# Optimization experiments

Hardware: AMD Instinct MI355X
Metric: run time of the kernel (lower is better)

Reference implementation:

```python
import jax, jax.numpy as jnp
import numpy as np

B, L, D, H = 2, 2048, 512, 8
HD = D // H  # head_dim used only for the concat/reshape trick


def setup_inputs() -> dict:
    key = jax.random.key(0)
    ks = jax.random.split(key, 7)
    s = 0.02  # small init so softmax isn't saturated
    return {
        "q": jax.random.normal(ks[0], (B, L, D), jnp.float32),
        "k": jax.random.normal(ks[1], (B, L, D), jnp.float32),
        "v": jax.random.normal(ks[2], (B, L, D), jnp.float32),
        # per-head full-width projections: W[h] is the nn.Linear weight [out,in]
        "Wq": jax.random.normal(ks[3], (H, D, D), jnp.float32) * s,
        "Wk": jax.random.normal(ks[4], (H, D, D), jnp.float32) * s,
        "Wv": jax.random.normal(ks[5], (H, D, D), jnp.float32) * s,
        # output_layer Linear(d_model*num_heads -> d_model, bias=False)
        "Wo": jax.random.normal(ks[6], (D, H * D), jnp.float32) * s,
    }


def reference(q, k, v, Wq, Wk, Wv, Wo):
    # Each head applies its own full d_model x d_model projections (Linear: x @ W^T)
    qh = jnp.einsum('bld,hed->bhle', q, Wq)  # [B,H,L,D]
    kh = jnp.einsum('bld,hed->bhle', k, Wk)
    vh = jnp.einsum('bld,hed->bhle', v, Wv)
    # scaled by sqrt(d_k) with d_k = d_model (as in the original code)
    scores = jnp.einsum('bhle,bhme->bhlm', qh, kh) / jnp.sqrt(jnp.float32(D))
    attn = jax.nn.softmax(scores, axis=-1)          # [B,H,L,L] (dropout = identity in eval)
    ctx = jnp.einsum('bhlm,bhme->bhle', attn, vh)   # [B,H,L,D]
    # torch: each head ctx [B,L,D] -> view(B,L,H,HD); cat over heads on last dim -> [B,L,H,H*HD]; flatten
    comb = ctx.reshape(B, H, L, H, HD).transpose(0, 2, 3, 1, 4).reshape(B, L, H * D)
    out = comb @ Wo.T                               # [B,L,D]
    return out, attn
```

## Files before the change

kernel.cpp:

```cpp
#include <hip/hip_runtime.h>
#include <cstdio>
#include <cstdint>


#define AS1 __attribute__((address_space(1)))
#define AS3 __attribute__((address_space(3)))

typedef __attribute__((ext_vector_type(8))) short bf16x8;
typedef __attribute__((ext_vector_type(4))) short short4v;
typedef __attribute__((ext_vector_type(4))) float f32x4;

constexpr int cB = 2, cH = 8, cL = 2048, cD = 512;
constexpr float SCORE_SCALE = 0.044194173824159216f;

__device__ __forceinline__ short f2bf(float f) {
  return __builtin_bit_cast(short, static_cast<__bf16>(f));
}

__device__ __forceinline__ void gload16(const void* g, void* l) {
  __builtin_amdgcn_global_load_lds((AS1 const void*)g, (AS3 void*)l, 16, 0, 0);
}

struct CvtArgs { const float4* s[7]; short4v* d[7]; };

__global__ __launch_bounds__(256) void cvt_all(CvtArgs a) {
  const int z = blockIdx.y;
  const int i = blockIdx.x * 256 + threadIdx.x;
  const float4 v = a.s[z][i];
  short4v o = { f2bf(v.x), f2bf(v.y), f2bf(v.z), f2bf(v.w) };
  a.d[z][i] = o;
}

enum { M_PROJ = 0, M_PROJV = 1, M_SCORES = 2, M_OUT = 3 };

template <int MODE>
__global__ __launch_bounds__(256) void gemm_nt(const short* __restrict__ Ap,
                                               const short* __restrict__ Bp,
                                               void* __restrict__ Cp,
                                               float2* __restrict__ Sp) {
  constexpr int K   = (MODE == M_OUT) ? 2048 : 512;
  constexpr int LDA = (MODE == M_OUT) ? 4096 : 512;
  constexpr int LDB = (MODE == M_OUT) ? 4096 : 512;

  __shared__ short As[128 * 32];
  __shared__ short Bs[128 * 32];

  const int t = threadIdx.x;
  const int lane = t & 63;
  const int wv = t >> 6;
  const int wm = wv >> 1, wn = wv & 1;
  const int z = blockIdx.z;

  size_t Aoff, Boff;
  if constexpr (MODE == M_PROJ || MODE == M_PROJV) {
    Aoff = (size_t)(z >> 3) * ((size_t)cL * cD);
    Boff = (size_t)(z & 7) * ((size_t)cD * cD);
  } else if constexpr (MODE == M_SCORES) {
    Aoff = (size_t)z * ((size_t)cL * cD);
    Boff = (size_t)z * ((size_t)cL * cD);
  } else {
    Aoff = (size_t)(z >> 1) * ((size_t)cL * 4096) + (size_t)(z & 1) * 2048;
    Boff = (size_t)(z & 1) * 2048;
  }

  const short* Ag0 = Ap + Aoff + (size_t)(blockIdx.y * 128) * LDA;
  const short* Bg0 = Bp + Boff + (size_t)(blockIdx.x * 128) * LDB;

  f32x4 acc[4][4];
#pragma unroll
  for (int i = 0; i < 4; ++i)
#pragma unroll
    for (int j = 0; j < 4; ++j) acc[i][j] = (f32x4){0.f, 0.f, 0.f, 0.f};

  for (int kt = 0; kt < K; kt += 32) {
    __syncthreads();
#pragma unroll
    for (int r = 0; r < 2; ++r) {
      const int cbase = r * 256 + wv * 64;
      const int c = cbase + lane;
      const int row = c >> 2, col = (c & 3) * 8;
      gload16(Ag0 + (size_t)row * LDA + kt + col, &As[cbase * 8]);
    }
#pragma unroll
    for (int r = 0; r < 2; ++r) {
      const int cbase = r * 256 + wv * 64;
      const int c = cbase + lane;
      const int row = c >> 2, col = (c & 3) * 8;
      gload16(Bg0 + (size_t)row * LDB + kt + col, &Bs[cbase * 8]);
    }
    __syncthreads();

    const int koff = (lane >> 4) * 8;
    const int ar = wm * 64 + (lane & 15);
    const int br = wn * 64 + (lane & 15);
    bf16x8 af[4], bfv[4];
#pragma unroll
    for (int i = 0; i < 4; ++i) af[i] = *(const bf16x8*)&As[(ar + i * 16) * 32 + koff];
#pragma unroll
    for (int j = 0; j < 4; ++j) bfv[j] = *(const bf16x8*)&Bs[(br + j * 16) * 32 + koff];
#pragma unroll
    for (int i = 0; i < 4; ++i)
#pragma unroll
      for (int j = 0; j < 4; ++j)
        acc[i][j] = __builtin_amdgcn_mfma_f32_16x16x32_bf16(af[i], bfv[j], acc[i][j], 0, 0, 0);
  }

  const int r0 = (lane >> 4) * 4;
  const int cc = lane & 15;
  const int rowbase = blockIdx.y * 128 + wm * 64 + r0;
  const int colbase = blockIdx.x * 128 + wn * 64 + cc;

  if constexpr (MODE == M_PROJ) {
    short* C = (short*)Cp + (size_t)z * ((size_t)cL * cD);
#pragma unroll
    for (int i = 0; i < 4; ++i)
#pragma unroll
      for (int j = 0; j < 4; ++j)
#pragma unroll
        for (int r = 0; r < 4; ++r)
          C[(size_t)(rowbase + i * 16 + r) * cD + (colbase + j * 16)] = f2bf(acc[i][j][r]);
  } else if constexpr (MODE == M_PROJV) {
    short* C = (short*)Cp + (size_t)z * ((size_t)cD * cL);
#pragma unroll
    for (int i = 0; i < 4; ++i)
#pragma unroll
      for (int j = 0; j < 4; ++j) {
        short4v o = { f2bf(acc[i][j][0]), f2bf(acc[i][j][1]),
                      f2bf(acc[i][j][2]), f2bf(acc[i][j][3]) };
        *(short4v*)&C[(size_t)(colbase + j * 16) * cL + (rowbase + i * 16)] = o;
      }
  } else if constexpr (MODE == M_SCORES) {
    float* C = (float*)Cp + (size_t)z * ((size_t)cL * cL);
    float2* ps = Sp + (size_t)z * ((size_t)cL * 32);
    const int pid = blockIdx.x * 2 + wn;
#pragma unroll
    for (int i = 0; i < 4; ++i) {
      float sv[4][4];
#pragma unroll
      for (int j = 0; j < 4; ++j)
#pragma unroll
        for (int r = 0; r < 4; ++r) sv[j][r] = acc[i][j][r] * SCORE_SCALE;
#pragma unroll
      for (int j = 0; j < 4; ++j)
#pragma unroll
        for (int r = 0; r < 4; ++r)
          C[(size_t)(rowbase + i * 16 + r) * cL + (colbase + j * 16)] = sv[j][r];
#pragma unroll
      for (int r = 0; r < 4; ++r) {
        float mx = fmaxf(fmaxf(sv[0][r], sv[1][r]), fmaxf(sv[2][r], sv[3][r]));
#pragma unroll
        for (int off = 1; off < 16; off <<= 1) mx = fmaxf(mx, __shfl_xor(mx, off, 64));
        float sm = __expf(sv[0][r] - mx) + __expf(sv[1][r] - mx) +
                   __expf(sv[2][r] - mx) + __expf(sv[3][r] - mx);
#pragma unroll
        for (int off = 1; off < 16; off <<= 1) sm += __shfl_xor(sm, off, 64);
        if ((lane & 15) == 0)
          ps[(size_t)(rowbase + i * 16 + r) * 32 + pid] = make_float2(mx, sm);
      }
    }
  } else {
    float* C = (float*)Cp + (size_t)((z & 1) * 2 + (z >> 1)) * ((size_t)cL * cD);
#pragma unroll
    for (int i = 0; i < 4; ++i)
#pragma unroll
      for (int j = 0; j < 4; ++j)
#pragma unroll
        for (int r = 0; r < 4; ++r)
          C[(size_t)(rowbase + i * 16 + r) * cD + (colbase + j * 16)] = acc[i][j][r];
  }
}

__global__ __launch_bounds__(256) void combine_stats(const float2* __restrict__ ps,
                                                     float2* __restrict__ stats) {
  const int row = blockIdx.x * 256 + threadIdx.x;
  const float2* p = ps + (size_t)row * 32;
  float m = -1e30f;
#pragma unroll
  for (int i = 0; i < 32; ++i) m = fmaxf(m, p[i].x);
  float l = 0.f;
#pragma unroll
  for (int i = 0; i < 32; ++i) l += p[i].y * __expf(p[i].x - m);
  stats[row] = make_float2(m, 1.0f / l);
}

__global__ __launch_bounds__(512) void fused_ctx(const short* __restrict__ vhT,
                                                 const float2* __restrict__ stats,
                                                 float* __restrict__ attn,
                                                 short* __restrict__ comb) {
  __shared__ short Bs[2][512 * 32];
  __shared__ short Pb[2][128 * 32];

  const int t = threadIdx.x;
  const int lane = t & 63;
  const int wv = t >> 6;
  const int wm = wv >> 2, wn = wv & 3;
  const int rowblk = blockIdx.x;
  const int z = blockIdx.y;

  const int trow = t >> 2;
  const int tcb = t & 3;
  const int tslot = tcb ^ ((trow >> 1) & 3);
  const int grow = rowblk * 128 + trow;
  float* sp = attn + ((size_t)z * cL + grow) * cL + tcb * 8;
  const float2 st = stats[(size_t)z * cL + grow];
  const float m = st.x, invl = st.y;

  const short* Bg = vhT + (size_t)z * ((size_t)cD * cL);

  f32x4 acc[4][8];
#pragma unroll
  for (int i = 0; i < 4; ++i)
#pragma unroll
    for (int j = 0; j < 8; ++j) acc[i][j] = (f32x4){0.f, 0.f, 0.f, 0.f};

  const int qk = lane >> 4;
  const int ar = wm * 64 + (lane & 15);
  const int br = wn * 128 + (lane & 15);

  auto stageB = [&](int nb, int kt) {
#pragma unroll
    for (int r = 0; r < 4; ++r) {
      const int cbase = r * 512 + wv * 64;
      const int c = cbase + lane;
      const int row = c >> 2;
      const int swcol = ((c & 3) ^ ((row >> 1) & 3)) * 8;
      gload16(Bg + (size_t)row * cL + kt + swcol, &Bs[nb][cbase * 8]);
    }
  };
  auto transform = [&](int ck, float4 v0, float4 v1) -> bf16x8 {
    float* dst = sp + ck * 32;
    const float p0 = __expf(v0.x - m) * invl;
    const float p1 = __expf(v0.y - m) * invl;
    const float p2 = __expf(v0.z - m) * invl;
    const float p3 = __expf(v0.w - m) * invl;
    const float p4 = __expf(v1.x - m) * invl;
    const float p5 = __expf(v1.y - m) * invl;
    const float p6 = __expf(v1.z - m) * invl;
    const float p7 = __expf(v1.w - m) * invl;
    *(float4*)(dst)     = make_float4(p0, p1, p2, p3);
    *(float4*)(dst + 4) = make_float4(p4, p5, p6, p7);
    bf16x8 pb = { f2bf(p0), f2bf(p1), f2bf(p2), f2bf(p3),
                  f2bf(p4), f2bf(p5), f2bf(p6), f2bf(p7) };
    return pb;
  };

  stageB(0, 0);
  float4 c0 = *(const float4*)(sp);
  float4 c1 = *(const float4*)(sp + 4);
  bf16x8 pb = transform(0, c0, c1);
  c0 = *(const float4*)(sp + 32);
  c1 = *(const float4*)(sp + 36);
  *(bf16x8*)&Pb[0][trow * 32 + tslot * 8] = pb;

  for (int k = 0; k < 63; ++k) {
    const int cb = k & 1, nb = cb ^ 1;
    pb = transform(k + 1, c0, c1);
    const int kc = (k + 2) & 63;
    c0 = *(const float4*)(sp + kc * 32);
    c1 = *(const float4*)(sp + kc * 32 + 4);
    asm volatile("s_waitcnt vmcnt(4) lgkmcnt(0)" ::: "memory");
    __builtin_amdgcn_sched_barrier(0);
    __builtin_amdgcn_s_barrier();
    __builtin_amdgcn_sched_barrier(0);
    *(bf16x8*)&Pb[nb][trow * 32 + tslot * 8] = pb;
    stageB(nb, (k + 1) * 32);
    __builtin_amdgcn_sched_barrier(0);
    bf16x8 af[4], bfv[8];
#pragma unroll
    for (int i = 0; i < 4; ++i) {
      const int rA = ar + i * 16;
      af[i] = *(const bf16x8*)&Pb[cb][rA * 32 + (qk ^ ((rA >> 1) & 3)) * 8];
    }
#pragma unroll
    for (int j = 0; j < 8; ++j) {
      const int rB = br + j * 16;
      bfv[j] = *(const bf16x8*)&Bs[cb][rB * 32 + (qk ^ ((rB >> 1) & 3)) * 8];
    }
    __builtin_amdgcn_s_setprio(1);
#pragma unroll
    for (int i = 0; i < 4; ++i)
#pragma unroll
      for (int j = 0; j < 8; ++j)
        acc[i][j] = __builtin_amdgcn_mfma_f32_16x16x32_bf16(af[i], bfv[j], acc[i][j], 0, 0, 0);
    __builtin_amdgcn_s_setprio(0);
  }

  asm volatile("s_waitcnt vmcnt(0) lgkmcnt(0)" ::: "memory");
  __builtin_amdgcn_sched_barrier(0);
  __builtin_amdgcn_s_barrier();
  __builtin_amdgcn_sched_barrier(0);
  {
    bf16x8 af[4], bfv[8];
#pragma unroll
    for (int i = 0; i < 4; ++i) {
      const int rA = ar + i * 16;
      af[i] = *(const bf16x8*)&Pb[1][rA * 32 + (qk ^ ((rA >> 1) & 3)) * 8];
    }
#pragma unroll
    for (int j = 0; j < 8; ++j) {
      const int rB = br + j * 16;
      bfv[j] = *(const bf16x8*)&Bs[1][rB * 32 + (qk ^ ((rB >> 1) & 3)) * 8];
    }
    __builtin_amdgcn_s_setprio(1);
#pragma unroll
    for (int i = 0; i < 4; ++i)
#pragma unroll
      for (int j = 0; j < 8; ++j)
        acc[i][j] = __builtin_amdgcn_mfma_f32_16x16x32_bf16(af[i], bfv[j], acc[i][j], 0, 0, 0);
    __builtin_amdgcn_s_setprio(0);
  }

  const int r0 = (lane >> 4) * 4;
  const int cc = lane & 15;
  short* C = comb + (size_t)(z >> 3) * ((size_t)cL * (cH * cD));
  const int h = z & 7;
  const int rowbase = rowblk * 128 + wm * 64 + r0;
#pragma unroll
  for (int i = 0; i < 4; ++i)
#pragma unroll
    for (int j = 0; j < 8; ++j) {
      const int e = wn * 128 + j * 16 + cc;
      const int jc = ((e >> 6) << 9) + (h << 6) + (e & 63);
#pragma unroll
      for (int r = 0; r < 4; ++r)
        C[(size_t)(rowbase + i * 16 + r) * (cH * cD) + jc] = f2bf(acc[i][j][r]);
    }
}

__global__ __launch_bounds__(256) void add_halves(const float4* __restrict__ p,
                                                  float4* __restrict__ out) {
  const int i = blockIdx.x * 256 + threadIdx.x;
  const float4 a = p[i];
  const float4 b = p[i + (cB * cL * cD) / 4];
  out[i] = make_float4(a.x + b.x, a.y + b.y, a.z + b.z, a.w + b.w);
}

extern "C" void kernel_launch(void* const* d_in, const int* in_sizes, int n_in,
                              void* d_out, int out_size, void* d_ws, size_t ws_size,
                              hipStream_t stream) {
  (void)in_sizes; (void)n_in; (void)out_size;

  const float* q  = (const float*)d_in[0];
  const float* k  = (const float*)d_in[1];
  const float* v  = (const float*)d_in[2];
  const float* Wq = (const float*)d_in[3];
  const float* Wk = (const float*)d_in[4];
  const float* Wv = (const float*)d_in[5];
  const float* Wo = (const float*)d_in[6];

  float* out  = (float*)d_out;
  float* attn = out + (size_t)cB * cL * cD;

  constexpr size_t Mi = 1ull << 20;
  char* ws = (char*)d_ws;
  short* qbf = (short*)(ws + 0 * Mi);
  short* kbf = (short*)(ws + 4 * Mi);
  short* vbf = (short*)(ws + 8 * Mi);
  short* wqb = (short*)(ws + 12 * Mi);
  short* wkb = (short*)(ws + 16 * Mi);
  short* wvb = (short*)(ws + 20 * Mi);
  short* wob = (short*)(ws + 24 * Mi);
  short* qh  = (short*)(ws + 28 * Mi);
  short* kh  = (short*)(ws + 60 * Mi);
  short* vhT = (short*)(ws + 92 * Mi);
  short* comb = qh;
  float2* stats  = (float2*)(ws + 0 * Mi);
  float2* pstats = (float2*)(ws + 4 * Mi);
  float*  pout   = (float*)(ws + 60 * Mi);

  if (ws_size < 124 * Mi) {
    fprintf(stderr, "kernel_launch: ws too small (%zu < %zu)\n", ws_size, 124 * Mi);
    return;
  }

  CvtArgs ca;
  ca.s[0] = (const float4*)q;  ca.d[0] = (short4v*)qbf;
  ca.s[1] = (const float4*)k;  ca.d[1] = (short4v*)kbf;
  ca.s[2] = (const float4*)v;  ca.d[2] = (short4v*)vbf;
  ca.s[3] = (const float4*)Wq; ca.d[3] = (short4v*)wqb;
  ca.s[4] = (const float4*)Wk; ca.d[4] = (short4v*)wkb;
  ca.s[5] = (const float4*)Wv; ca.d[5] = (short4v*)wvb;
  ca.s[6] = (const float4*)Wo; ca.d[6] = (short4v*)wob;
  cvt_all<<<dim3(2048, 7), 256, 0, stream>>>(ca);

  gemm_nt<M_PROJ ><<<dim3(4, 16, 16), 256, 0, stream>>>(qbf, wqb, qh, nullptr);
  gemm_nt<M_PROJ ><<<dim3(4, 16, 16), 256, 0, stream>>>(kbf, wkb, kh, nullptr);
  gemm_nt<M_PROJV><<<dim3(4, 16, 16), 256, 0, stream>>>(vbf, wvb, vhT, nullptr);

  gemm_nt<M_SCORES><<<dim3(16, 16, 16), 256, 0, stream>>>(qh, kh, attn, pstats);

  combine_stats<<<cB * cH * cL / 256, 256, 0, stream>>>(pstats, stats);

  fused_ctx<<<dim3(16, cB * cH), 512, 0, stream>>>(vhT, stats, attn, comb);

  gemm_nt<M_OUT><<<dim3(4, 16, 4), 256, 0, stream>>>(comb, wob, (void*)pout, nullptr);

  add_halves<<<2048, 256, 0, stream>>>((const float4*)pout, (float4*)out);
}
```

Measured before the change: 773.0 us.

## Triple-buffer GEMM loads, halve fused_ctx row tile, split output GEMM K four ways

The generic NT GEMM moves from a single-buffered, double-sync loop to a three-stage LDS ring. Loads are issued two tiles ahead and guarded by vmcnt waits and a single barrier per step, so global latency overlaps the MFMA work. The fused softmax-times-V kernel now handles 64 rows per block instead of 128, which doubles the grid to 512 blocks and halves per-wave accumulators to raise occupancy. The output projection is split-K four ways instead of two, giving twice as many blocks at the cost of a larger partial buffer and a four-way reduction kernel.

```diff
diff --git a/kernel.cpp b/kernel.cpp
--- a/kernel.cpp
+++ b/kernel.cpp
@@ -38,12 +38,12 @@
                                                const short* __restrict__ Bp,
                                                void* __restrict__ Cp,
                                                float2* __restrict__ Sp) {
-  constexpr int K   = (MODE == M_OUT) ? 2048 : 512;
+  constexpr int K   = (MODE == M_OUT) ? 1024 : 512;
   constexpr int LDA = (MODE == M_OUT) ? 4096 : 512;
   constexpr int LDB = (MODE == M_OUT) ? 4096 : 512;
 
-  __shared__ short As[128 * 32];
-  __shared__ short Bs[128 * 32];
+  __shared__ short As[3][128 * 32];
+  __shared__ short Bs[3][128 * 32];
 
   const int t = threadIdx.x;
   const int lane = t & 63;
@@ -59,8 +59,8 @@
     Aoff = (size_t)z * ((size_t)cL * cD);
     Boff = (size_t)z * ((size_t)cL * cD);
   } else {
-    Aoff = (size_t)(z >> 1) * ((size_t)cL * 4096) + (size_t)(z & 1) * 2048;
-    Boff = (size_t)(z & 1) * 2048;
+    Aoff = (size_t)(z >> 2) * ((size_t)cL * 4096) + (size_t)(z & 3) * 1024;
+    Boff = (size_t)(z & 3) * 1024;
   }
 
   const short* Ag0 = Ap + Aoff + (size_t)(blockIdx.y * 128) * LDA;
@@ -72,37 +72,54 @@
 #pragma unroll
     for (int j = 0; j < 4; ++j) acc[i][j] = (f32x4){0.f, 0.f, 0.f, 0.f};
 
-  for (int kt = 0; kt < K; kt += 32) {
-    __syncthreads();
+  auto stage = [&](int b, int kt) {
 #pragma unroll
     for (int r = 0; r < 2; ++r) {
       const int cbase = r * 256 + wv * 64;
       const int c = cbase + lane;
       const int row = c >> 2, col = (c & 3) * 8;
-      gload16(Ag0 + (size_t)row * LDA + kt + col, &As[cbase * 8]);
+      gload16(Ag0 + (size_t)row * LDA + kt + col, &As[b][cbase * 8]);
     }
 #pragma unroll
     for (int r = 0; r < 2; ++r) {
       const int cbase = r * 256 + wv * 64;
       const int c = cbase + lane;
       const int row = c >> 2, col = (c & 3) * 8;
-      gload16(Bg0 + (size_t)row * LDB + kt + col, &Bs[cbase * 8]);
-    }
-    __syncthreads();
-
-    const int koff = (lane >> 4) * 8;
-    const int ar = wm * 64 + (lane & 15);
-    const int br = wn * 64 + (lane & 15);
+      gload16(Bg0 + (size_t)row * LDB + kt + col, &Bs[b][cbase * 8]);
+    }
+  };
+
+  const int koff = (lane >> 4) * 8;
+  const int ar = wm * 64 + (lane & 15);
+  const int br = wn * 64 + (lane & 15);
+
+  constexpr int nt = K / 32;
+  stage(0, 0);
+  stage(1, 32);
+  int cur = 0, pre = 2;
+  for (int tt = 0; tt < nt; ++tt) {
+    if (tt < nt - 1) { asm volatile("s_waitcnt vmcnt(4) lgkmcnt(0)" ::: "memory"); }
+    else             { asm volatile("s_waitcnt vmcnt(0) lgkmcnt(0)" ::: "memory"); }
+    __builtin_amdgcn_sched_barrier(0);
+    __builtin_amdgcn_s_barrier();
+    __builtin_amdgcn_sched_barrier(0);
+    if (tt + 2 < nt) stage(pre, (tt + 2) * 32);
+    __builtin_amdgcn_sched_barrier(0);
+
     bf16x8 af[4], bfv[4];
 #pragma unroll
-    for (int i = 0; i < 4; ++i) af[i] = *(const bf16x8*)&As[(ar + i * 16) * 32 + koff];
-#pragma unroll
-    for (int j = 0; j < 4; ++j) bfv[j] = *(const bf16x8*)&Bs[(br + j * 16) * 32 + koff];
+    for (int i = 0; i < 4; ++i) af[i] = *(const bf16x8*)&As[cur][(ar + i * 16) * 32 + koff];
+#pragma unroll
+    for (int j = 0; j < 4; ++j) bfv[j] = *(const bf16x8*)&Bs[cur][(br + j * 16) * 32 + koff];
+    __builtin_amdgcn_s_setprio(1);
 #pragma unroll
     for (int i = 0; i < 4; ++i)
 #pragma unroll
       for (int j = 0; j < 4; ++j)
         acc[i][j] = __builtin_amdgcn_mfma_f32_16x16x32_bf16(af[i], bfv[j], acc[i][j], 0, 0, 0);
+    __builtin_amdgcn_s_setprio(0);
+    cur = (cur == 2) ? 0 : cur + 1;
+    pre = (pre == 2) ? 0 : pre + 1;
   }
 
   const int r0 = (lane >> 4) * 4;
@@ -159,7 +176,7 @@
       }
     }
   } else {
-    float* C = (float*)Cp + (size_t)((z & 1) * 2 + (z >> 1)) * ((size_t)cL * cD);
+    float* C = (float*)Cp + (size_t)((z & 3) * 2 + (z >> 2)) * ((size_t)cL * cD);
 #pragma unroll
     for (int i = 0; i < 4; ++i)
 #pragma unroll
@@ -183,39 +200,38 @@
   stats[row] = make_float2(m, 1.0f / l);
 }
 
-__global__ __launch_bounds__(512) void fused_ctx(const short* __restrict__ vhT,
-                                                 const float2* __restrict__ stats,
-                                                 float* __restrict__ attn,
-                                                 short* __restrict__ comb) {
+__global__ __launch_bounds__(512, 4) void fused_ctx(const short* __restrict__ vhT,
+                                                    const float2* __restrict__ stats,
+                                                    float* __restrict__ attn,
+                                                    short* __restrict__ comb) {
   __shared__ short Bs[2][512 * 32];
-  __shared__ short Pb[2][128 * 32];
+  __shared__ short Pb[2][64 * 32];
 
   const int t = threadIdx.x;
   const int lane = t & 63;
   const int wv = t >> 6;
-  const int wm = wv >> 2, wn = wv & 3;
   const int rowblk = blockIdx.x;
   const int z = blockIdx.y;
 
-  const int trow = t >> 2;
-  const int tcb = t & 3;
-  const int tslot = tcb ^ ((trow >> 1) & 3);
-  const int grow = rowblk * 128 + trow;
-  float* sp = attn + ((size_t)z * cL + grow) * cL + tcb * 8;
+  const int trow = t >> 3;
+  const int tcb = t & 7;
+  const int pidx = trow * 32 + (((tcb >> 1) ^ ((trow >> 1) & 3)) << 3) + ((tcb & 1) << 2);
+  const int grow = rowblk * 64 + trow;
+  float* sp = attn + ((size_t)z * cL + grow) * cL + tcb * 4;
   const float2 st = stats[(size_t)z * cL + grow];
   const float m = st.x, invl = st.y;
 
   const short* Bg = vhT + (size_t)z * ((size_t)cD * cL);
 
-  f32x4 acc[4][8];
+  f32x4 acc[4][4];
 #pragma unroll
   for (int i = 0; i < 4; ++i)
 #pragma unroll
-    for (int j = 0; j < 8; ++j) acc[i][j] = (f32x4){0.f, 0.f, 0.f, 0.f};
+    for (int j = 0; j < 4; ++j) acc[i][j] = (f32x4){0.f, 0.f, 0.f, 0.f};
 
   const int qk = lane >> 4;
-  const int ar = wm * 64 + (lane & 15);
-  const int br = wn * 128 + (lane & 15);
+  const int arr = lane & 15;
+  const int br = wv * 64 + (lane & 15);
 
   auto stageB = [&](int nb, int kt) {
 #pragma unroll
@@ -227,60 +243,51 @@
       gload16(Bg + (size_t)row * cL + kt + swcol, &Bs[nb][cbase * 8]);
     }
   };
-  auto transform = [&](int ck, float4 v0, float4 v1) -> bf16x8 {
+  auto transform = [&](int ck, float4 v) -> short4v {
     float* dst = sp + ck * 32;
-    const float p0 = __expf(v0.x - m) * invl;
-    const float p1 = __expf(v0.y - m) * invl;
-    const float p2 = __expf(v0.z - m) * invl;
-    const float p3 = __expf(v0.w - m) * invl;
-    const float p4 = __expf(v1.x - m) * invl;
-    const float p5 = __expf(v1.y - m) * invl;
-    const float p6 = __expf(v1.z - m) * invl;
-    const float p7 = __expf(v1.w - m) * invl;
-    *(float4*)(dst)     = make_float4(p0, p1, p2, p3);
-    *(float4*)(dst + 4) = make_float4(p4, p5, p6, p7);
-    bf16x8 pb = { f2bf(p0), f2bf(p1), f2bf(p2), f2bf(p3),
-                  f2bf(p4), f2bf(p5), f2bf(p6), f2bf(p7) };
+    const float p0 = __expf(v.x - m) * invl;
+    const float p1 = __expf(v.y - m) * invl;
+    const float p2 = __expf(v.z - m) * invl;
+    const float p3 = __expf(v.w - m) * invl;
+    *(float4*)dst = make_float4(p0, p1, p2, p3);
+    short4v pb = { f2bf(p0), f2bf(p1), f2bf(p2), f2bf(p3) };
     return pb;
   };
 
   stageB(0, 0);
-  float4 c0 = *(const float4*)(sp);
-  float4 c1 = *(const float4*)(sp + 4);
-  bf16x8 pb = transform(0, c0, c1);
-  c0 = *(const float4*)(sp + 32);
-  c1 = *(const float4*)(sp + 36);
-  *(bf16x8*)&Pb[0][trow * 32 + tslot * 8] = pb;
+  float4 c = *(const float4*)(sp);
+  short4v pb = transform(0, c);
+  c = *(const float4*)(sp + 32);
+  *(short4v*)&Pb[0][pidx] = pb;
 
   for (int k = 0; k < 63; ++k) {
     const int cb = k & 1, nb = cb ^ 1;
-    pb = transform(k + 1, c0, c1);
+    pb = transform(k + 1, c);
     const int kc = (k + 2) & 63;
-    c0 = *(const float4*)(sp + kc * 32);
-    c1 = *(const float4*)(sp + kc * 32 + 4);
-    asm volatile("s_waitcnt vmcnt(4) lgkmcnt(0)" ::: "memory");
+    c = *(const float4*)(sp + kc * 32);
+    asm volatile("s_waitcnt vmcnt(2) lgkmcnt(0)" ::: "memory");
     __builtin_amdgcn_sched_barrier(0);
     __builtin_amdgcn_s_barrier();
     __builtin_amdgcn_sched_barrier(0);
-    *(bf16x8*)&Pb[nb][trow * 32 + tslot * 8] = pb;
+    *(short4v*)&Pb[nb][pidx] = pb;
     stageB(nb, (k + 1) * 32);
     __builtin_amdgcn_sched_barrier(0);
-    bf16x8 af[4], bfv[8];
+    bf16x8 af[4], bfv[4];
 #pragma unroll
     for (int i = 0; i < 4; ++i) {
-      const int rA = ar + i * 16;
-      af[i] = *(const bf16x8*)&Pb[cb][rA * 32 + (qk ^ ((rA >> 1) & 3)) * 8];
-    }
-#pragma unroll
-    for (int j = 0; j < 8; ++j) {
+      const int rA = arr + i * 16;
+      af[i] = *(const bf16x8*)&Pb[cb][rA * 32 + ((qk ^ ((rA >> 1) & 3)) << 3)];
+    }
+#pragma unroll
+    for (int j = 0; j < 4; ++j) {
       const int rB = br + j * 16;
-      bfv[j] = *(const bf16x8*)&Bs[cb][rB * 32 + (qk ^ ((rB >> 1) & 3)) * 8];
+      bfv[j] = *(const bf16x8*)&Bs[cb][rB * 32 + ((qk ^ ((rB >> 1) & 3)) << 3)];
     }
     __builtin_amdgcn_s_setprio(1);
 #pragma unroll
     for (int i = 0; i < 4; ++i)
 #pragma unroll
-      for (int j = 0; j < 8; ++j)
+      for (int j = 0; j < 4; ++j)
         acc[i][j] = __builtin_amdgcn_mfma_f32_16x16x32_bf16(af[i], bfv[j], acc[i][j], 0, 0, 0);
     __builtin_amdgcn_s_setprio(0);
   }
@@ -290,22 +297,22 @@
   __builtin_amdgcn_s_barrier();
   __builtin_amdgcn_sched_barrier(0);
   {
-    bf16x8 af[4], bfv[8];
+    bf16x8 af[4], bfv[4];
 #pragma unroll
     for (int i = 0; i < 4; ++i) {
-      const int rA = ar + i * 16;
-      af[i] = *(const bf16x8*)&Pb[1][rA * 32 + (qk ^ ((rA >> 1) & 3)) * 8];
-    }
-#pragma unroll
-    for (int j = 0; j < 8; ++j) {
+      const int rA = arr + i * 16;
+      af[i] = *(const bf16x8*)&Pb[1][rA * 32 + ((qk ^ ((rA >> 1) & 3)) << 3)];
+    }
+#pragma unroll
+    for (int j = 0; j < 4; ++j) {
       const int rB = br + j * 16;
-      bfv[j] = *(const bf16x8*)&Bs[1][rB * 32 + (qk ^ ((rB >> 1) & 3)) * 8];
+      bfv[j] = *(const bf16x8*)&Bs[1][rB * 32 + ((qk ^ ((rB >> 1) & 3)) << 3)];
     }
     __builtin_amdgcn_s_setprio(1);
 #pragma unroll
     for (int i = 0; i < 4; ++i)
 #pragma unroll
-      for (int j = 0; j < 8; ++j)
+      for (int j = 0; j < 4; ++j)
         acc[i][j] = __builtin_amdgcn_mfma_f32_16x16x32_bf16(af[i], bfv[j], acc[i][j], 0, 0, 0);
     __builtin_amdgcn_s_setprio(0);
   }
@@ -314,12 +321,12 @@
   const int cc = lane & 15;
   short* C = comb + (size_t)(z >> 3) * ((size_t)cL * (cH * cD));
   const int h = z & 7;
-  const int rowbase = rowblk * 128 + wm * 64 + r0;
+  const int rowbase = rowblk * 64 + r0;
 #pragma unroll
   for (int i = 0; i < 4; ++i)
 #pragma unroll
-    for (int j = 0; j < 8; ++j) {
-      const int e = wn * 128 + j * 16 + cc;
+    for (int j = 0; j < 4; ++j) {
+      const int e = wv * 64 + j * 16 + cc;
       const int jc = ((e >> 6) << 9) + (h << 6) + (e & 63);
 #pragma unroll
       for (int r = 0; r < 4; ++r)
@@ -327,12 +334,13 @@
     }
 }
 
-__global__ __launch_bounds__(256) void add_halves(const float4* __restrict__ p,
-                                                  float4* __restrict__ out) {
+__global__ __launch_bounds__(256) void add_quads(const float4* __restrict__ p,
+                                                 float4* __restrict__ out) {
   const int i = blockIdx.x * 256 + threadIdx.x;
-  const float4 a = p[i];
-  const float4 b = p[i + (cB * cL * cD) / 4];
-  out[i] = make_float4(a.x + b.x, a.y + b.y, a.z + b.z, a.w + b.w);
+  constexpr int S = (cB * cL * cD) / 4;
+  const float4 a = p[i], b = p[i + S], c = p[i + 2 * S], d = p[i + 3 * S];
+  out[i] = make_float4(a.x + b.x + c.x + d.x, a.y + b.y + c.y + d.y,
+                       a.z + b.z + c.z + d.z, a.w + b.w + c.w + d.w);
 }
 
 extern "C" void kernel_launch(void* const* d_in, const int* in_sizes, int n_in,
@@ -391,9 +399,9 @@
 
   combine_stats<<<cB * cH * cL / 256, 256, 0, stream>>>(pstats, stats);
 
-  fused_ctx<<<dim3(16, cB * cH), 512, 0, stream>>>(vhT, stats, attn, comb);
-
-  gemm_nt<M_OUT><<<dim3(4, 16, 4), 256, 0, stream>>>(comb, wob, (void*)pout, nullptr);
-
-  add_halves<<<2048, 256, 0, stream>>>((const float4*)pout, (float4*)out);
-}
+  fused_ctx<<<dim3(32, cB * cH), 512, 0, stream>>>(vhT, stats, attn, comb);
+
+  gemm_nt<M_OUT><<<dim3(4, 16, 8), 256, 0, stream>>>(comb, wob, (void*)pout, nullptr);
+
+  add_quads<<<2048, 256, 0, stream>>>((const float4*)pout, (float4*)out);
+}
```

Result: faster. 740.5 us (-4.2%).
